# Optimization experiments

Measured on AMD Instinct MI355X. Metric: run time of the kernel, lower is better.

Reference implementation:

```python
import jax, jax.numpy as jnp
import numpy as np

SEQ, H, NC = 20, 128, 100000

def _lstm_cell(x, h, c, Wih, Whh, bih, bhh):
    # gates: [B, 4H] in PyTorch order i, f, g, o
    g = x @ Wih.T + bih + h @ Whh.T + bhh
    i, f, gg, o = jnp.split(g, 4, axis=-1)
    c2 = jax.nn.sigmoid(f) * c + jax.nn.sigmoid(i) * jnp.tanh(gg)
    h2 = jax.nn.sigmoid(o) * jnp.tanh(c2)
    return h2, c2

def setup_inputs() -> dict:
    key = jax.random.key(0)
    ks = jax.random.split(key, 24)
    u = lambda k, shp, bound: jax.random.uniform(k, shp, jnp.float32, -bound, bound)
    s1 = 1.0 / np.sqrt(H)       # PyTorch LSTMCell init bound, hidden_size=H
    s2 = 1.0 / np.sqrt(2 * H)   # combined cell, hidden_size=2H
    kn = lambda k, shp: jax.random.normal(k, shp, jnp.float32) * np.sqrt(2.0 / shp[1])  # kaiming_normal_
    return {
        'x': jax.random.normal(ks[0], (SEQ, 1, H), jnp.float32),
        'h0f': kn(ks[1], (1, H)), 'c0f': kn(ks[2], (1, H)),
        'h0b': kn(ks[3], (1, H)), 'c0b': kn(ks[4], (1, H)),
        'h0l': kn(ks[5], (1, 2 * H)), 'c0l': kn(ks[6], (1, 2 * H)),
        'Wih_f': u(ks[7], (4 * H, H), s1), 'Whh_f': u(ks[8], (4 * H, H), s1),
        'bih_f': u(ks[9], (4 * H,), s1), 'bhh_f': u(ks[10], (4 * H,), s1),
        'Wih_b': u(ks[11], (4 * H, H), s1), 'Whh_b': u(ks[12], (4 * H, H), s1),
        'bih_b': u(ks[13], (4 * H,), s1), 'bhh_b': u(ks[14], (4 * H,), s1),
        'Wih_l': u(ks[15], (8 * H, 2 * H), s2), 'Whh_l': u(ks[16], (8 * H, 2 * H), s2),
        'bih_l': u(ks[17], (8 * H,), s2), 'bhh_l': u(ks[18], (8 * H,), s2),
        'Wlin': u(ks[19], (NC, 2 * H), 1.0 / np.sqrt(2 * H)),
        'blin': u(ks[20], (NC,), 1.0 / np.sqrt(2 * H)),
    }

def reference(x, h0f, c0f, h0b, c0b, h0l, c0l,
              Wih_f, Whh_f, bih_f, bhh_f,
              Wih_b, Whh_b, bih_b, bhh_b,
              Wih_l, Whh_l, bih_l, bhh_l,
              Wlin, blin):
    xs = x.reshape(SEQ, 1, H)

    def step_f(carry, xt):
        h, c = _lstm_cell(xt, carry[0], carry[1], Wih_f, Whh_f, bih_f, bhh_f)
        return (h, c), h
    _, fwd = jax.lax.scan(step_f, (h0f, c0f), xs)          # [SEQ, 1, H]

    def step_b(carry, xt):
        h, c = _lstm_cell(xt, carry[0], carry[1], Wih_b, Whh_b, bih_b, bhh_b)
        return (h, c), h
    # backward list is kept in reversed-scan order (NOT flipped back), per source zip
    _, bwd = jax.lax.scan(step_b, (h0b, c0b), xs[::-1])    # [SEQ, 1, H]

    comb = jnp.concatenate([fwd, bwd], axis=-1)            # [SEQ, 1, 2H]

    def step_l(carry, xt):
        h, c = _lstm_cell(xt, carry[0], carry[1], Wih_l, Whh_l, bih_l, bhh_l)
        return (h, c), h
    _, hl = jax.lax.scan(step_l, (h0l, c0l), comb)         # [SEQ, 1, 2H]

    fb = hl.reshape(SEQ, 2 * H)
    return fb @ Wlin.T + blin                              # [SEQ, NC]
```

## Files before the change

kernel.cpp:

```cpp
#include <hip/hip_runtime.h>
#include <stdint.h>

#define SEQ  20
#define H1   128
#define H2   256
#define NCLS 100000

__device__ __forceinline__ float sigm(float x) { return 1.0f / (1.0f + __expf(-x)); }
__device__ __forceinline__ float tanhfast(float x) {
    float e = __expf(-2.0f * fabsf(x));
    float t = (1.0f - e) / (1.0f + e);
    return copysignf(t, x);
}

__global__ __launch_bounds__(1024, 4) void k_l1(
    const float* __restrict__ x,
    const float* __restrict__ h0f, const float* __restrict__ c0f,
    const float* __restrict__ h0b, const float* __restrict__ c0b,
    const float* __restrict__ WihF, const float* __restrict__ WhhF,
    const float* __restrict__ bihF, const float* __restrict__ bhhF,
    const float* __restrict__ WihB, const float* __restrict__ WhhB,
    const float* __restrict__ bihB, const float* __restrict__ bhhB,
    float* __restrict__ comb)
{
    const int dir = blockIdx.x;
    const float* Wih = dir ? WihB : WihF;
    const float* Whh = dir ? WhhB : WhhF;
    const float* bih = dir ? bihB : bihF;
    const float* bhh = dir ? bhhB : bhhF;
    const float* h0  = dir ? h0b  : h0f;
    const float* c0  = dir ? c0b  : c0f;

    __shared__ float xs[SEQ * H1];
    __shared__ float hcur[H1];
    __shared__ float biasL[4 * H1];
    __shared__ float gxs[4 * H1][SEQ + 1];
    __shared__ float partial[4 * 520];

    const int tid = threadIdx.x;
    const int cg  = tid >> 8;
    const int rp  = tid & 255;
    const int r0  = rp * 2;

    for (int i = tid; i < SEQ * H1; i += 1024) xs[i] = x[i];
    if (tid < 4 * H1) biasL[tid] = bih[tid] + bhh[tid];
    if (tid < H1) hcur[tid] = h0[tid];
    float creg = (tid < H1) ? c0[tid] : 0.0f;

    float4 wa[8], wb[8];
    {
        const float4* pa = (const float4*)(Wih + r0 * H1 + cg * 32);
        const float4* pb = (const float4*)(Wih + (r0 + 1) * H1 + cg * 32);
#pragma unroll
        for (int j = 0; j < 8; ++j) { wa[j] = pa[j]; wb[j] = pb[j]; }
    }
    __syncthreads();

    for (int t = 0; t < SEQ; ++t) {
        const float4* xp = (const float4*)(xs + (dir ? (SEQ - 1 - t) : t) * H1 + cg * 32);
        float a0 = 0.f, a1 = 0.f;
#pragma unroll
        for (int j = 0; j < 8; ++j) {
            float4 v = xp[j];
            a0 += wa[j].x * v.x + wa[j].y * v.y + wa[j].z * v.z + wa[j].w * v.w;
            a1 += wb[j].x * v.x + wb[j].y * v.y + wb[j].z * v.z + wb[j].w * v.w;
        }
        *(float2*)(partial + cg * 520 + r0) = make_float2(a0, a1);
        __syncthreads();
        if (tid < 4 * H1) {
            float s = biasL[tid] + partial[tid] + partial[520 + tid]
                    + partial[1040 + tid] + partial[1560 + tid];
            gxs[tid][t] = s;
        }
        __syncthreads();
    }

    {
        const float4* pa = (const float4*)(Whh + r0 * H1 + cg * 32);
        const float4* pb = (const float4*)(Whh + (r0 + 1) * H1 + cg * 32);
#pragma unroll
        for (int j = 0; j < 8; ++j) { wa[j] = pa[j]; wb[j] = pb[j]; }
    }

    for (int t = 0; t < SEQ; ++t) {
        const float4* hp = (const float4*)(hcur + cg * 32);
        float a0 = 0.f, a1 = 0.f;
#pragma unroll
        for (int j = 0; j < 8; ++j) {
            float4 v = hp[j];
            a0 += wa[j].x * v.x + wa[j].y * v.y + wa[j].z * v.z + wa[j].w * v.w;
            a1 += wb[j].x * v.x + wb[j].y * v.y + wb[j].z * v.z + wb[j].w * v.w;
        }
        *(float2*)(partial + cg * 520 + r0) = make_float2(a0, a1);
        __syncthreads();
        if (tid < H1) {
            const int c = tid;
            float s[4];
#pragma unroll
            for (int g = 0; g < 4; ++g) {
                float acc = gxs[g * H1 + c][t];
#pragma unroll
                for (int q = 0; q < 4; ++q) acc += partial[q * 520 + g * H1 + c];
                s[g] = acc;
            }
            float cn = sigm(s[1]) * creg + sigm(s[0]) * tanhfast(s[2]);
            creg = cn;
            float hn = sigm(s[3]) * tanhfast(cn);
            comb[t * H2 + dir * H1 + c] = hn;
            hcur[c] = hn;
        }
        __syncthreads();
    }
}

__global__ __launch_bounds__(1024, 4) void k_l2(
    const float* __restrict__ Whhl,
    const float* __restrict__ h0l, const float* __restrict__ c0l,
    const float* __restrict__ Wihl,
    const float* __restrict__ bihl, const float* __restrict__ bhhl,
    const float* __restrict__ comb,
    float* __restrict__ fb,
    float* __restrict__ hg2,
    int* __restrict__ flags)
{
    const int b = blockIdx.x;
    __shared__ float cs[SEQ * H2];
    __shared__ float hcur[H2];
    __shared__ float biasL[H2];
    __shared__ float gxs[H2][SEQ + 1];
    __shared__ float partial[8 * 260];

    const int tid = threadIdx.x;
    const int cg  = tid >> 7;
    const int rp  = tid & 127;
    const int L0  = rp * 2;
    const int R0  = (L0 >> 6) * H2 + b * 64 + (L0 & 63);

    for (int i = tid; i < SEQ * H2; i += 1024) cs[i] = comb[i];
    if (tid < H2) {
        int g = tid >> 6, c = tid & 63;
        int R = g * H2 + b * 64 + c;
        biasL[tid] = bihl[R] + bhhl[R];
        hcur[tid]  = h0l[tid];
    }
    float creg = (tid < 64) ? c0l[b * 64 + tid] : 0.0f;

    float4 wa[8], wb[8];
    {
        const float4* pa = (const float4*)(Wihl + (size_t)R0 * H2 + cg * 32);
        const float4* pb = (const float4*)(Wihl + (size_t)(R0 + 1) * H2 + cg * 32);
#pragma unroll
        for (int j = 0; j < 8; ++j) { wa[j] = pa[j]; wb[j] = pb[j]; }
    }
    __syncthreads();

    for (int t = 0; t < SEQ; ++t) {
        const float4* cp = (const float4*)(cs + t * H2 + cg * 32);
        float a0 = 0.f, a1 = 0.f;
#pragma unroll
        for (int j = 0; j < 8; ++j) {
            float4 v = cp[j];
            a0 += wa[j].x * v.x + wa[j].y * v.y + wa[j].z * v.z + wa[j].w * v.w;
            a1 += wb[j].x * v.x + wb[j].y * v.y + wb[j].z * v.z + wb[j].w * v.w;
        }
        *(float2*)(partial + cg * 260 + L0) = make_float2(a0, a1);
        __syncthreads();
        if (tid < H2) {
            float s = biasL[tid];
#pragma unroll
            for (int q = 0; q < 8; ++q) s += partial[q * 260 + tid];
            gxs[tid][t] = s;
        }
        __syncthreads();
    }

    {
        const float4* pa = (const float4*)(Whhl + (size_t)R0 * H2 + cg * 32);
        const float4* pb = (const float4*)(Whhl + (size_t)(R0 + 1) * H2 + cg * 32);
#pragma unroll
        for (int j = 0; j < 8; ++j) { wa[j] = pa[j]; wb[j] = pb[j]; }
    }

    for (int t = 0; t < SEQ; ++t) {
        const float4* hp = (const float4*)(hcur + cg * 32);
        float a0 = 0.f, a1 = 0.f;
#pragma unroll
        for (int j = 0; j < 8; ++j) {
            float4 v = hp[j];
            a0 += wa[j].x * v.x + wa[j].y * v.y + wa[j].z * v.z + wa[j].w * v.w;
            a1 += wb[j].x * v.x + wb[j].y * v.y + wb[j].z * v.z + wb[j].w * v.w;
        }
        *(float2*)(partial + cg * 260 + L0) = make_float2(a0, a1);
        __syncthreads();

        if (tid < 64) {
            const int c = tid;
            float s[4];
#pragma unroll
            for (int g = 0; g < 4; ++g) {
                float acc = gxs[g * 64 + c][t];
#pragma unroll
                for (int q = 0; q < 8; ++q) acc += partial[q * 260 + g * 64 + c];
                s[g] = acc;
            }
            float cn = sigm(s[1]) * creg + sigm(s[0]) * tanhfast(s[2]);
            creg = cn;
            float hn = sigm(s[3]) * tanhfast(cn);
            fb[t * H2 + b * 64 + c] = hn;
            hcur[b * 64 + c] = hn;
            if (t + 1 < SEQ) {
                __hip_atomic_store(&hg2[b * 64 + c], hn,
                                   __ATOMIC_RELAXED, __HIP_MEMORY_SCOPE_AGENT);
                __threadfence();
                if (tid == 0)
                    __hip_atomic_store(&flags[b], t + 1,
                                       __ATOMIC_RELEASE, __HIP_MEMORY_SCOPE_AGENT);
            }
        } else if (tid < 256 && t + 1 < SEQ) {
            const int idx = (b * 64 + tid) & 255;
            const int sh  = idx >> 6;
            while (__hip_atomic_load(&flags[sh], __ATOMIC_ACQUIRE,
                                     __HIP_MEMORY_SCOPE_AGENT) <= t)
                __builtin_amdgcn_s_sleep(1);
            hcur[idx] = __hip_atomic_load(&hg2[idx],
                                          __ATOMIC_RELAXED, __HIP_MEMORY_SCOPE_AGENT);
        }
        __syncthreads();
    }
}

__global__ __launch_bounds__(256, 4) void k_out_v(
    const float* __restrict__ Wlin, const float* __restrict__ blin,
    const float* __restrict__ fb, float* __restrict__ out)
{
    __shared__ float fbs[H2][SEQ];
    const int tid = threadIdx.x;
    for (int t = 0; t < SEQ; ++t) fbs[tid][t] = fb[t * H2 + tid];
    __syncthreads();

    int n = blockIdx.x * 256 + tid;
    if (n >= NCLS) return;
    float acc[SEQ];
    float bv = blin[n];
#pragma unroll
    for (int t = 0; t < SEQ; ++t) acc[t] = bv;

    const float* wp = Wlin + (size_t)n * H2;
    for (int k = 0; k < H2; k += 4) {
        float4 wv = *(const float4*)(wp + k);
#pragma unroll
        for (int t = 0; t < SEQ; t += 4) {
            float4 f0 = *(const float4*)(&fbs[k][t]);
            float4 f1 = *(const float4*)(&fbs[k + 1][t]);
            float4 f2 = *(const float4*)(&fbs[k + 2][t]);
            float4 f3 = *(const float4*)(&fbs[k + 3][t]);
            acc[t]     += wv.x * f0.x + wv.y * f1.x + wv.z * f2.x + wv.w * f3.x;
            acc[t + 1] += wv.x * f0.y + wv.y * f1.y + wv.z * f2.y + wv.w * f3.y;
            acc[t + 2] += wv.x * f0.z + wv.y * f1.z + wv.z * f2.z + wv.w * f3.z;
            acc[t + 3] += wv.x * f0.w + wv.y * f1.w + wv.z * f2.w + wv.w * f3.w;
        }
    }
#pragma unroll
    for (int t = 0; t < SEQ; ++t)
        out[(size_t)t * NCLS + n] = acc[t];
}

extern "C" void kernel_launch(void* const* d_in, const int* in_sizes, int n_in,
                              void* d_out, int out_size, void* d_ws, size_t ws_size,
                              hipStream_t stream)
{
    const float* x    = (const float*)d_in[0];
    const float* h0f_ = (const float*)d_in[1];
    const float* c0f_ = (const float*)d_in[2];
    const float* h0b_ = (const float*)d_in[3];
    const float* c0b_ = (const float*)d_in[4];
    const float* h0l_ = (const float*)d_in[5];
    const float* c0l_ = (const float*)d_in[6];
    const float* WihF = (const float*)d_in[7];
    const float* WhhF = (const float*)d_in[8];
    const float* bihF = (const float*)d_in[9];
    const float* bhhF = (const float*)d_in[10];
    const float* WihB = (const float*)d_in[11];
    const float* WhhB = (const float*)d_in[12];
    const float* bihB = (const float*)d_in[13];
    const float* bhhB = (const float*)d_in[14];
    const float* Wihl = (const float*)d_in[15];
    const float* Whhl = (const float*)d_in[16];
    const float* bihl = (const float*)d_in[17];
    const float* bhhl = (const float*)d_in[18];
    const float* Wlin = (const float*)d_in[19];
    const float* blin = (const float*)d_in[20];

    char* ws = (char*)d_ws;
    int*   flags = (int*)ws;
    float* hg2   = (float*)(ws + 1536);
    float* comb  = (float*)(ws + 4096);
    float* fb    = (float*)(ws + 24576);

    hipMemsetAsync(flags, 0, 256, stream);

    k_l1<<<2, 1024, 0, stream>>>(x, h0f_, c0f_, h0b_, c0b_,
                                 WihF, WhhF, bihF, bhhF,
                                 WihB, WhhB, bihB, bhhB,
                                 comb);
    k_l2<<<4, 1024, 0, stream>>>(Whhl, h0l_, c0l_,
                                 Wihl, bihl, bhhl,
                                 comb, fb, hg2, flags);
    k_out_v<<<391, 256, 0, stream>>>(Wlin, blin, fb, (float*)d_out);
}
```

Baseline: 354.3 us.

## Fuse all LSTM layers and output projection into one persistent flag-synchronized kernel

Replaces three kernel launches with one grid in which two blocks run the bidirectional first layer, eight blocks run the second layer per timestep as soon as first-layer outputs are flagged, and the remaining blocks compute the output projection. The second layer is pipelined against the first through per-timestep release/acquire flags instead of waiting for the whole first layer. The output blocks prefetch their Wlin rows into cache while they wait. This removes launch gaps and serial layer dependency, but relies on every block being co-resident and adds spin-wait overhead. Output blocks now use 1024 threads each.

```diff
diff --git a/kernel.cpp b/kernel.cpp
--- a/kernel.cpp
+++ b/kernel.cpp
@@ -5,6 +5,13 @@
 #define H1   128
 #define H2   256
 #define NCLS 100000
+#define NOUTB 98
+#define GRID (10 + NOUTB)
+
+#define AQ  __ATOMIC_ACQUIRE
+#define RL  __ATOMIC_RELEASE
+#define RX  __ATOMIC_RELAXED
+#define AG  __HIP_MEMORY_SCOPE_AGENT
 
 __device__ __forceinline__ float sigm(float x) { return 1.0f / (1.0f + __expf(-x)); }
 __device__ __forceinline__ float tanhfast(float x) {
@@ -13,7 +20,8 @@
     return copysignf(t, x);
 }
 
-__global__ __launch_bounds__(1024, 4) void k_l1(
+__global__ __launch_bounds__(1024) __attribute__((amdgpu_waves_per_eu(4, 4)))
+void k_fused(
     const float* __restrict__ x,
     const float* __restrict__ h0f, const float* __restrict__ c0f,
     const float* __restrict__ h0b, const float* __restrict__ c0b,
@@ -21,248 +29,234 @@
     const float* __restrict__ bihF, const float* __restrict__ bhhF,
     const float* __restrict__ WihB, const float* __restrict__ WhhB,
     const float* __restrict__ bihB, const float* __restrict__ bhhB,
-    float* __restrict__ comb)
+    const float* __restrict__ Wihl, const float* __restrict__ Whhl,
+    const float* __restrict__ bihl, const float* __restrict__ bhhl,
+    const float* __restrict__ h0l,  const float* __restrict__ c0l,
+    const float* __restrict__ Wlin, const float* __restrict__ blin,
+    float* __restrict__ comb, float* __restrict__ fb,
+    float* __restrict__ hg2, int* __restrict__ flags,
+    float* __restrict__ out)
 {
-    const int dir = blockIdx.x;
-    const float* Wih = dir ? WihB : WihF;
-    const float* Whh = dir ? WhhB : WhhF;
-    const float* bih = dir ? bihB : bihF;
-    const float* bhh = dir ? bhhB : bhhF;
-    const float* h0  = dir ? h0b  : h0f;
-    const float* c0  = dir ? c0b  : c0f;
-
-    __shared__ float xs[SEQ * H1];
-    __shared__ float hcur[H1];
-    __shared__ float biasL[4 * H1];
-    __shared__ float gxs[4 * H1][SEQ + 1];
-    __shared__ float partial[4 * 520];
-
+    const int b   = blockIdx.x;
     const int tid = threadIdx.x;
-    const int cg  = tid >> 8;
-    const int rp  = tid & 255;
-    const int r0  = rp * 2;
-
-    for (int i = tid; i < SEQ * H1; i += 1024) xs[i] = x[i];
-    if (tid < 4 * H1) biasL[tid] = bih[tid] + bhh[tid];
-    if (tid < H1) hcur[tid] = h0[tid];
-    float creg = (tid < H1) ? c0[tid] : 0.0f;
-
-    float4 wa[8], wb[8];
-    {
-        const float4* pa = (const float4*)(Wih + r0 * H1 + cg * 32);
-        const float4* pb = (const float4*)(Wih + (r0 + 1) * H1 + cg * 32);
-#pragma unroll
-        for (int j = 0; j < 8; ++j) { wa[j] = pa[j]; wb[j] = pb[j]; }
-    }
-    __syncthreads();
-
-    for (int t = 0; t < SEQ; ++t) {
-        const float4* xp = (const float4*)(xs + (dir ? (SEQ - 1 - t) : t) * H1 + cg * 32);
-        float a0 = 0.f, a1 = 0.f;
-#pragma unroll
-        for (int j = 0; j < 8; ++j) {
-            float4 v = xp[j];
-            a0 += wa[j].x * v.x + wa[j].y * v.y + wa[j].z * v.z + wa[j].w * v.w;
-            a1 += wb[j].x * v.x + wb[j].y * v.y + wb[j].z * v.z + wb[j].w * v.w;
-        }
-        *(float2*)(partial + cg * 520 + r0) = make_float2(a0, a1);
+
+    if (b < 2) {
+        const int dir = b;
+        const float* Wih = dir ? WihB : WihF;
+        const float* Whh = dir ? WhhB : WhhF;
+        const float* bih = dir ? bihB : bihF;
+        const float* bhh = dir ? bhhB : bhhF;
+        const float* h0  = dir ? h0b  : h0f;
+        const float* c0  = dir ? c0b  : c0f;
+
+        __shared__ float xs[SEQ * H1];
+        __shared__ float hcur[H1];
+        __shared__ float biasL[4 * H1];
+        __shared__ float gxs[4 * H1][SEQ + 1];
+        __shared__ float partial[4 * 520];
+
+        for (int i = tid; i < SEQ * H1; i += 1024) xs[i] = x[i];
+        if (tid < 4 * H1) biasL[tid] = bih[tid] + bhh[tid];
+        if (tid < H1) hcur[tid] = h0[tid];
+        float cregA = 0.f, cregB = 0.f;
+        if (tid < 64) { cregA = c0[tid]; cregB = c0[tid + 64]; }
+
+        const int pr = tid >> 1, ph = tid & 1;
+        {
+            float4 wf[16];
+            const float4* p = (const float4*)(Wih + pr * H1 + ph * 64);
+#pragma unroll
+            for (int j = 0; j < 16; ++j) wf[j] = p[j];
+            __syncthreads();
+            for (int t = 0; t < SEQ; ++t) {
+                const int tx = dir ? (SEQ - 1 - t) : t;
+                const float4* xp = (const float4*)(xs + tx * H1 + ph * 64);
+                float a = 0.f;
+#pragma unroll
+                for (int j = 0; j < 16; ++j) {
+                    float4 v = xp[j];
+                    a += wf[j].x * v.x + wf[j].y * v.y + wf[j].z * v.z + wf[j].w * v.w;
+                }
+                a += __shfl_xor(a, 1);
+                if (ph == 0) gxs[pr][t] = a + biasL[pr];
+            }
+        }
+        asm volatile("" ::: "memory");
+
+        const int cg = tid >> 8, rp = tid & 255, r0 = rp * 2;
+        float4 wa[8], wb[8];
+        {
+            const float4* pa = (const float4*)(Whh + r0 * H1 + cg * 32);
+            const float4* pb = (const float4*)(Whh + (r0 + 1) * H1 + cg * 32);
+#pragma unroll
+            for (int j = 0; j < 8; ++j) { wa[j] = pa[j]; wb[j] = pb[j]; }
+        }
         __syncthreads();
-        if (tid < 4 * H1) {
-            float s = biasL[tid] + partial[tid] + partial[520 + tid]
-                    + partial[1040 + tid] + partial[1560 + tid];
-            gxs[tid][t] = s;
-        }
+
+        for (int t = 0; t < SEQ; ++t) {
+            const float4* hp = (const float4*)(hcur + cg * 32);
+            float a0 = 0.f, a1 = 0.f;
+#pragma unroll
+            for (int j = 0; j < 8; ++j) {
+                float4 v = hp[j];
+                a0 += wa[j].x * v.x + wa[j].y * v.y + wa[j].z * v.z + wa[j].w * v.w;
+                a1 += wb[j].x * v.x + wb[j].y * v.y + wb[j].z * v.z + wb[j].w * v.w;
+            }
+            *(float2*)(partial + cg * 520 + r0) = make_float2(a0, a1);
+            __syncthreads();
+            if (tid < 64) {
+                const int c = tid;
+                float s0[4], s1[4];
+#pragma unroll
+                for (int g = 0; g < 4; ++g) {
+                    float accA = gxs[g * H1 + c][t];
+                    float accB = gxs[g * H1 + c + 64][t];
+#pragma unroll
+                    for (int q = 0; q < 4; ++q) {
+                        accA += partial[q * 520 + g * H1 + c];
+                        accB += partial[q * 520 + g * H1 + c + 64];
+                    }
+                    s0[g] = accA; s1[g] = accB;
+                }
+                float cnA = sigm(s0[1]) * cregA + sigm(s0[0]) * tanhfast(s0[2]);
+                float cnB = sigm(s1[1]) * cregB + sigm(s1[0]) * tanhfast(s1[2]);
+                cregA = cnA; cregB = cnB;
+                float hA = sigm(s0[3]) * tanhfast(cnA);
+                float hB = sigm(s1[3]) * tanhfast(cnB);
+                hcur[c] = hA; hcur[c + 64] = hB;
+                __hip_atomic_store(&comb[t * H2 + dir * H1 + c],      hA, RX, AG);
+                __hip_atomic_store(&comb[t * H2 + dir * H1 + c + 64], hB, RX, AG);
+                __threadfence();
+                if (tid == 0)
+                    __hip_atomic_store(&flags[dir * 32], t + 1, RL, AG);
+            }
+            __syncthreads();
+        }
+    } else if (b < 10) {
+        const int s = b - 2;
+        __shared__ float ct[H2];
+        __shared__ float hc2[H2];
+        __shared__ float bias2[128];
+        __shared__ float part2[8 * 132];
+
+        const int cg = tid >> 7;
+        const int L  = tid & 127;
+        const int R  = (L >> 5) * H2 + s * 32 + (L & 31);
+
+        float4 wih[8], whh[8];
+        {
+            const float4* pi = (const float4*)(Wihl + (size_t)R * H2 + cg * 32);
+            const float4* pw = (const float4*)(Whhl + (size_t)R * H2 + cg * 32);
+#pragma unroll
+            for (int j = 0; j < 8; ++j) { wih[j] = pi[j]; whh[j] = pw[j]; }
+        }
+        if (tid < 128) bias2[tid] = bihl[R] + bhhl[R];
+        if (tid < H2)  hc2[tid] = h0l[tid];
+        float creg = (tid < 32) ? c0l[s * 32 + tid] : 0.0f;
         __syncthreads();
-    }
-
-    {
-        const float4* pa = (const float4*)(Whh + r0 * H1 + cg * 32);
-        const float4* pb = (const float4*)(Whh + (r0 + 1) * H1 + cg * 32);
-#pragma unroll
-        for (int j = 0; j < 8; ++j) { wa[j] = pa[j]; wb[j] = pb[j]; }
-    }
-
-    for (int t = 0; t < SEQ; ++t) {
-        const float4* hp = (const float4*)(hcur + cg * 32);
-        float a0 = 0.f, a1 = 0.f;
-#pragma unroll
-        for (int j = 0; j < 8; ++j) {
-            float4 v = hp[j];
-            a0 += wa[j].x * v.x + wa[j].y * v.y + wa[j].z * v.z + wa[j].w * v.w;
-            a1 += wb[j].x * v.x + wb[j].y * v.y + wb[j].z * v.z + wb[j].w * v.w;
-        }
-        *(float2*)(partial + cg * 520 + r0) = make_float2(a0, a1);
-        __syncthreads();
-        if (tid < H1) {
-            const int c = tid;
-            float s[4];
-#pragma unroll
-            for (int g = 0; g < 4; ++g) {
-                float acc = gxs[g * H1 + c][t];
-#pragma unroll
-                for (int q = 0; q < 4; ++q) acc += partial[q * 520 + g * H1 + c];
-                s[g] = acc;
-            }
-            float cn = sigm(s[1]) * creg + sigm(s[0]) * tanhfast(s[2]);
-            creg = cn;
-            float hn = sigm(s[3]) * tanhfast(cn);
-            comb[t * H2 + dir * H1 + c] = hn;
-            hcur[c] = hn;
-        }
-        __syncthreads();
-    }
-}
-
-__global__ __launch_bounds__(1024, 4) void k_l2(
-    const float* __restrict__ Whhl,
-    const float* __restrict__ h0l, const float* __restrict__ c0l,
-    const float* __restrict__ Wihl,
-    const float* __restrict__ bihl, const float* __restrict__ bhhl,
-    const float* __restrict__ comb,
-    float* __restrict__ fb,
-    float* __restrict__ hg2,
-    int* __restrict__ flags)
-{
-    const int b = blockIdx.x;
-    __shared__ float cs[SEQ * H2];
-    __shared__ float hcur[H2];
-    __shared__ float biasL[H2];
-    __shared__ float gxs[H2][SEQ + 1];
-    __shared__ float partial[8 * 260];
-
-    const int tid = threadIdx.x;
-    const int cg  = tid >> 7;
-    const int rp  = tid & 127;
-    const int L0  = rp * 2;
-    const int R0  = (L0 >> 6) * H2 + b * 64 + (L0 & 63);
-
-    for (int i = tid; i < SEQ * H2; i += 1024) cs[i] = comb[i];
-    if (tid < H2) {
-        int g = tid >> 6, c = tid & 63;
-        int R = g * H2 + b * 64 + c;
-        biasL[tid] = bihl[R] + bhhl[R];
-        hcur[tid]  = h0l[tid];
-    }
-    float creg = (tid < 64) ? c0l[b * 64 + tid] : 0.0f;
-
-    float4 wa[8], wb[8];
-    {
-        const float4* pa = (const float4*)(Wihl + (size_t)R0 * H2 + cg * 32);
-        const float4* pb = (const float4*)(Wihl + (size_t)(R0 + 1) * H2 + cg * 32);
-#pragma unroll
-        for (int j = 0; j < 8; ++j) { wa[j] = pa[j]; wb[j] = pb[j]; }
-    }
-    __syncthreads();
-
-    for (int t = 0; t < SEQ; ++t) {
-        const float4* cp = (const float4*)(cs + t * H2 + cg * 32);
-        float a0 = 0.f, a1 = 0.f;
-#pragma unroll
-        for (int j = 0; j < 8; ++j) {
-            float4 v = cp[j];
-            a0 += wa[j].x * v.x + wa[j].y * v.y + wa[j].z * v.z + wa[j].w * v.w;
-            a1 += wb[j].x * v.x + wb[j].y * v.y + wb[j].z * v.z + wb[j].w * v.w;
-        }
-        *(float2*)(partial + cg * 260 + L0) = make_float2(a0, a1);
+
+        for (int t = 0; t < SEQ; ++t) {
+            if (tid < 64) {
+                while (true) {
+                    int f0 = __hip_atomic_load(&flags[0],  AQ, AG);
+                    int f1 = __hip_atomic_load(&flags[32], AQ, AG);
+                    if (f0 > t && f1 > t) break;
+                    __builtin_amdgcn_s_sleep(1);
+                }
+#pragma unroll
+                for (int j = 0; j < 4; ++j)
+                    ct[tid * 4 + j] = __hip_atomic_load(&comb[t * H2 + tid * 4 + j], RX, AG);
+            }
+            __syncthreads();
+            {
+                const float4* cp = (const float4*)(ct  + cg * 32);
+                const float4* hp = (const float4*)(hc2 + cg * 32);
+                float a = 0.f;
+#pragma unroll
+                for (int j = 0; j < 8; ++j) {
+                    float4 cv = cp[j], hv = hp[j];
+                    a += wih[j].x * cv.x + wih[j].y * cv.y + wih[j].z * cv.z + wih[j].w * cv.w
+                       + whh[j].x * hv.x + whh[j].y * hv.y + whh[j].z * hv.z + whh[j].w * hv.w;
+                }
+                part2[cg * 132 + L] = a;
+            }
+            __syncthreads();
+            if (tid < 32) {
+                float sg[4];
+#pragma unroll
+                for (int g = 0; g < 4; ++g) {
+                    float acc = bias2[g * 32 + tid];
+#pragma unroll
+                    for (int q = 0; q < 8; ++q) acc += part2[q * 132 + g * 32 + tid];
+                    sg[g] = acc;
+                }
+                float cn = sigm(sg[1]) * creg + sigm(sg[0]) * tanhfast(sg[2]);
+                creg = cn;
+                float hn = sigm(sg[3]) * tanhfast(cn);
+                hc2[s * 32 + tid] = hn;
+                __hip_atomic_store(&fb[t * H2 + s * 32 + tid],  hn, RX, AG);
+                __hip_atomic_store(&hg2[s * 32 + tid],          hn, RX, AG);
+                __threadfence();
+                if (tid == 0)
+                    __hip_atomic_store(&flags[(2 + s) * 32], t + 1, RL, AG);
+            } else if (tid >= 64 && tid < 288) {
+                const int idx = (s * 32 + tid - 32) & 255;
+                const int sh  = idx >> 5;
+                while (__hip_atomic_load(&flags[(2 + sh) * 32], AQ, AG) <= t)
+                    __builtin_amdgcn_s_sleep(1);
+                hc2[idx] = __hip_atomic_load(&hg2[idx], RX, AG);
+            }
+            __syncthreads();
+        }
+    } else {
+        const int ob = b - 10;
+        const int n  = ob * 1024 + tid;
+        __shared__ __align__(16) float fbs[H2][SEQ];
+
+        float keep = 0.f;
+        if (n < NCLS) {
+            const float4* wp4 = (const float4*)(Wlin + (size_t)n * H2);
+#pragma unroll
+            for (int j = 0; j < 64; j += 4) keep += wp4[j].x;
+        }
+        asm volatile("" :: "v"(keep));
+
+        if (tid < 8) {
+            while (__hip_atomic_load(&flags[(2 + tid) * 32], AQ, AG) < SEQ)
+                __builtin_amdgcn_s_sleep(4);
+        }
         __syncthreads();
         if (tid < H2) {
-            float s = biasL[tid];
-#pragma unroll
-            for (int q = 0; q < 8; ++q) s += partial[q * 260 + tid];
-            gxs[tid][t] = s;
+            for (int t = 0; t < SEQ; ++t)
+                fbs[tid][t] = __hip_atomic_load(&fb[t * H2 + tid], RX, AG);
         }
         __syncthreads();
+        if (n >= NCLS) return;
+
+        float acc[SEQ];
+        float bv = blin[n];
+#pragma unroll
+        for (int t = 0; t < SEQ; ++t) acc[t] = bv;
+
+        const float* wp = Wlin + (size_t)n * H2;
+        for (int k = 0; k < H2; k += 4) {
+            float4 wv = *(const float4*)(wp + k);
+#pragma unroll
+            for (int t = 0; t < SEQ; t += 4) {
+                float4 f0 = *(const float4*)(&fbs[k][t]);
+                float4 f1 = *(const float4*)(&fbs[k + 1][t]);
+                float4 f2 = *(const float4*)(&fbs[k + 2][t]);
+                float4 f3 = *(const float4*)(&fbs[k + 3][t]);
+                acc[t]     += wv.x * f0.x + wv.y * f1.x + wv.z * f2.x + wv.w * f3.x;
+                acc[t + 1] += wv.x * f0.y + wv.y * f1.y + wv.z * f2.y + wv.w * f3.y;
+                acc[t + 2] += wv.x * f0.z + wv.y * f1.z + wv.z * f2.z + wv.w * f3.z;
+                acc[t + 3] += wv.x * f0.w + wv.y * f1.w + wv.z * f2.w + wv.w * f3.w;
+            }
+        }
+#pragma unroll
+        for (int t = 0; t < SEQ; ++t)
+            out[(size_t)t * NCLS + n] = acc[t];
     }
-
-    {
-        const float4* pa = (const float4*)(Whhl + (size_t)R0 * H2 + cg * 32);
-        const float4* pb = (const float4*)(Whhl + (size_t)(R0 + 1) * H2 + cg * 32);
-#pragma unroll
-        for (int j = 0; j < 8; ++j) { wa[j] = pa[j]; wb[j] = pb[j]; }
-    }
-
-    for (int t = 0; t < SEQ; ++t) {
-        const float4* hp = (const float4*)(hcur + cg * 32);
-        float a0 = 0.f, a1 = 0.f;
-#pragma unroll
-        for (int j = 0; j < 8; ++j) {
-            float4 v = hp[j];
-            a0 += wa[j].x * v.x + wa[j].y * v.y + wa[j].z * v.z + wa[j].w * v.w;
-            a1 += wb[j].x * v.x + wb[j].y * v.y + wb[j].z * v.z + wb[j].w * v.w;
-        }
-        *(float2*)(partial + cg * 260 + L0) = make_float2(a0, a1);
-        __syncthreads();
-
-        if (tid < 64) {
-            const int c = tid;
-            float s[4];
-#pragma unroll
-            for (int g = 0; g < 4; ++g) {
-                float acc = gxs[g * 64 + c][t];
-#pragma unroll
-                for (int q = 0; q < 8; ++q) acc += partial[q * 260 + g * 64 + c];
-                s[g] = acc;
-            }
-            float cn = sigm(s[1]) * creg + sigm(s[0]) * tanhfast(s[2]);
-            creg = cn;
-            float hn = sigm(s[3]) * tanhfast(cn);
-            fb[t * H2 + b * 64 + c] = hn;
-            hcur[b * 64 + c] = hn;
-            if (t + 1 < SEQ) {
-                __hip_atomic_store(&hg2[b * 64 + c], hn,
-                                   __ATOMIC_RELAXED, __HIP_MEMORY_SCOPE_AGENT);
-                __threadfence();
-                if (tid == 0)
-                    __hip_atomic_store(&flags[b], t + 1,
-                                       __ATOMIC_RELEASE, __HIP_MEMORY_SCOPE_AGENT);
-            }
-        } else if (tid < 256 && t + 1 < SEQ) {
-            const int idx = (b * 64 + tid) & 255;
-            const int sh  = idx >> 6;
-            while (__hip_atomic_load(&flags[sh], __ATOMIC_ACQUIRE,
-                                     __HIP_MEMORY_SCOPE_AGENT) <= t)
-                __builtin_amdgcn_s_sleep(1);
-            hcur[idx] = __hip_atomic_load(&hg2[idx],
-                                          __ATOMIC_RELAXED, __HIP_MEMORY_SCOPE_AGENT);
-        }
-        __syncthreads();
-    }
-}
-
-__global__ __launch_bounds__(256, 4) void k_out_v(
-    const float* __restrict__ Wlin, const float* __restrict__ blin,
-    const float* __restrict__ fb, float* __restrict__ out)
-{
-    __shared__ float fbs[H2][SEQ];
-    const int tid = threadIdx.x;
-    for (int t = 0; t < SEQ; ++t) fbs[tid][t] = fb[t * H2 + tid];
-    __syncthreads();
-
-    int n = blockIdx.x * 256 + tid;
-    if (n >= NCLS) return;
-    float acc[SEQ];
-    float bv = blin[n];
-#pragma unroll
-    for (int t = 0; t < SEQ; ++t) acc[t] = bv;
-
-    const float* wp = Wlin + (size_t)n * H2;
-    for (int k = 0; k < H2; k += 4) {
-        float4 wv = *(const float4*)(wp + k);
-#pragma unroll
-        for (int t = 0; t < SEQ; t += 4) {
-            float4 f0 = *(const float4*)(&fbs[k][t]);
-            float4 f1 = *(const float4*)(&fbs[k + 1][t]);
-            float4 f2 = *(const float4*)(&fbs[k + 2][t]);
-            float4 f3 = *(const float4*)(&fbs[k + 3][t]);
-            acc[t]     += wv.x * f0.x + wv.y * f1.x + wv.z * f2.x + wv.w * f3.x;
-            acc[t + 1] += wv.x * f0.y + wv.y * f1.y + wv.z * f2.y + wv.w * f3.y;
-            acc[t + 2] += wv.x * f0.z + wv.y * f1.z + wv.z * f2.z + wv.w * f3.z;
-            acc[t + 3] += wv.x * f0.w + wv.y * f1.w + wv.z * f2.w + wv.w * f3.w;
-        }
-    }
-#pragma unroll
-    for (int t = 0; t < SEQ; ++t)
-        out[(size_t)t * NCLS + n] = acc[t];
 }
 
 extern "C" void kernel_launch(void* const* d_in, const int* in_sizes, int n_in,
@@ -293,18 +287,17 @@
 
     char* ws = (char*)d_ws;
     int*   flags = (int*)ws;
-    float* hg2   = (float*)(ws + 1536);
+    float* hg2   = (float*)(ws + 2048);
     float* comb  = (float*)(ws + 4096);
     float* fb    = (float*)(ws + 24576);
 
-    hipMemsetAsync(flags, 0, 256, stream);
-
-    k_l1<<<2, 1024, 0, stream>>>(x, h0f_, c0f_, h0b_, c0b_,
-                                 WihF, WhhF, bihF, bhhF,
-                                 WihB, WhhB, bihB, bhhB,
-                                 comb);
-    k_l2<<<4, 1024, 0, stream>>>(Whhl, h0l_, c0l_,
-                                 Wihl, bihl, bhhl,
-                                 comb, fb, hg2, flags);
-    k_out_v<<<391, 256, 0, stream>>>(Wlin, blin, fb, (float*)d_out);
+    hipMemsetAsync(flags, 0, 2048, stream);
+
+    k_fused<<<GRID, 1024, 0, stream>>>(
+        x, h0f_, c0f_, h0b_, c0b_,
+        WihF, WhhF, bihF, bhhF,
+        WihB, WhhB, bihB, bhhB,
+        Wihl, Whhl, bihl, bhhl,
+        h0l_, c0l_, Wlin, blin,
+        comb, fb, hg2, flags, (float*)d_out);
 }
```

New measurement: 535.2 us. 51.1% more time.
